# Performance work log

Hardware: AMD Instinct MI355X
Metric: run time of the kernel (lower is better)

Reference implementation:

```python
import jax, jax.numpy as jnp
import numpy as np

D_MODEL = 1024
N_HEADS = 16
D_HEAD = D_MODEL // N_HEADS
B, L = 4, 2048
NEG_INF = float('-inf')


def setup_inputs() -> dict:
    key = jax.random.key(0)
    ks = jax.random.split(key, 8)
    x = jax.random.normal(ks[0], (B, L, D_MODEL), dtype=jnp.float32)
    # sorted cumulative event times in hours (~0-2000h span)
    timestamps = jnp.cumsum(jax.random.uniform(ks[1], (B, L), dtype=jnp.float32), axis=-1)
    mask = jnp.ones((B, L), dtype=jnp.float32)
    s = 1.0 / np.sqrt(D_MODEL)
    W_qkv = jax.random.normal(ks[2], (3 * D_MODEL, D_MODEL), dtype=jnp.float32) * s
    b_qkv = jnp.zeros((3 * D_MODEL,), dtype=jnp.float32)
    W_out = jax.random.normal(ks[3], (D_MODEL, D_MODEL), dtype=jnp.float32) * s
    b_out = jnp.zeros((D_MODEL,), dtype=jnp.float32)
    decay_rate = jnp.full((N_HEADS,), 0.01, dtype=jnp.float32)
    return {"x": x, "timestamps": timestamps, "mask": mask,
            "W_qkv": W_qkv, "b_qkv": b_qkv, "W_out": W_out, "b_out": b_out,
            "decay_rate": decay_rate}


def reference(x, timestamps, mask, W_qkv, b_qkv, W_out, b_out, decay_rate):
    Bb, Ll, Dd = x.shape
    H, dh = N_HEADS, D_HEAD
    scale = dh ** (-0.5)
    qkv = x @ W_qkv.T + b_qkv                     # (B,L,3D)
    qkv = qkv.reshape(Bb, Ll, 3, H, dh).transpose(2, 0, 3, 1, 4)  # (3,B,H,L,dh)
    q, k, v = qkv[0], qkv[1], qkv[2]
    attn = jnp.einsum('bhqd,bhkd->bhqk', q, k) * scale
    t_diff = jnp.abs(timestamps[:, :, None] - timestamps[:, None, :])[:, None]  # (B,1,L,L)
    decay = jax.nn.softplus(decay_rate)[None, :, None, None]                    # (1,H,1,1)
    attn = attn - decay * t_diff / 24.0
    causal = jnp.triu(jnp.ones((Ll, Ll), dtype=bool), k=1)        # (L,L) True above diag
    attn = jnp.where(causal[None, None], NEG_INF, attn)
    pad = (mask == 0.0)[:, None, None, :]                         # (B,1,1,L) True=pad key
    attn = jnp.where(pad, NEG_INF, attn)
    attn = jax.nn.softmax(attn, axis=-1)
    out = jnp.einsum('bhqk,bhkd->bhqd', attn, v)                  # (B,H,L,dh)
    out = out.transpose(0, 2, 1, 3).reshape(Bb, Ll, Dd)
    return out @ W_out.T + b_out
```

## Files before the change

### kernel.cpp

```cpp
#include <hip/hip_runtime.h>
#include <stdint.h>
#include <math.h>

#define B_   4
#define L_   2048
#define H_   16
#define DH_  64
#define DM_  1024

typedef __bf16 bf16;
typedef __attribute__((ext_vector_type(8))) __bf16 bf16x8;
typedef __attribute__((ext_vector_type(4))) float f32x4;
typedef __attribute__((ext_vector_type(4))) int i32x4;
typedef __attribute__((ext_vector_type(4))) short s16x4;
typedef unsigned short u16;
typedef unsigned int u32;
typedef __attribute__((ext_vector_type(2))) unsigned int u32x2;
typedef __attribute__((ext_vector_type(4))) unsigned short u16x4;

typedef unsigned int u32g __attribute__((address_space(1)));
typedef unsigned int u32l __attribute__((address_space(3)));

__device__ __forceinline__ u16 f2bf(float f) {
  return __builtin_bit_cast(u16, (bf16)f);
}

__device__ __forceinline__ float exp2_fast(float x) {
  float r; asm("v_exp_f32 %0, %1" : "=v"(r) : "v"(x)); return r;
}

__device__ __forceinline__ void gload16(const void* g, void* l) {
  __builtin_amdgcn_global_load_lds((const u32g*)g, (u32l*)l, 16, 0, 0);
}

__device__ __forceinline__ f32x4 mfma16(s16x4 a, s16x4 b, f32x4 c) {
#if __has_builtin(__builtin_amdgcn_mfma_f32_16x16x16bf16_1k)
  return __builtin_amdgcn_mfma_f32_16x16x16bf16_1k(a, b, c, 0, 0, 0);
#else
  asm volatile("v_mfma_f32_16x16x16_bf16 %0, %1, %2, %0\n\ts_nop 7\n\ts_nop 2"
               : "+v"(c) : "v"(a), "v"(b));
  return c;
#endif
}

__global__ __launch_bounds__(256) void cvt_f32_bf16(const float* __restrict__ src,
                                                    u16* __restrict__ dst, int n4) {
  int i = blockIdx.x * 256 + threadIdx.x;
  if (i >= n4) return;
  f32x4 v = ((const f32x4*)src)[i];
  u16x4 o;
  o[0] = f2bf(v[0]); o[1] = f2bf(v[1]); o[2] = f2bf(v[2]); o[3] = f2bf(v[3]);
  ((u16x4*)dst)[i] = o;
}

__global__ __launch_bounds__(256) void bias_fill(const float* __restrict__ ts,
                                                 const float* __restrict__ msk,
                                                 const float* __restrict__ decay,
                                                 float* __restrict__ Bk) {
  int i = blockIdx.x * 256 + threadIdx.x;
  int bh = i >> 11, l = i & (L_ - 1);
  int b = bh >> 4, h = bh & 15;
  float dc24 = log1pf(__expf(decay[h])) * (1.0f / 24.0f) * 1.44269504f;
  float tv = ts[b * L_ + l], mv = msk[b * L_ + l];
  Bk[i] = (mv != 0.f) ? dc24 * tv : -INFINITY;
}

__global__ __launch_bounds__(256) void gemm_bf16(
    const u16* __restrict__ A, const u16* __restrict__ Bm, const float* __restrict__ bias,
    int M, int N, int K, int mode,
    u16* __restrict__ Qb, u16* __restrict__ Kb, u16* __restrict__ Vt, float* __restrict__ Cout)
{
  extern __shared__ char smem[];
  u16* ltr = (u16*)smem;

  const int tid = threadIdx.x;
  const int m0 = blockIdx.y * 128, n0 = blockIdx.x * 128;
  const int lane = tid & 63, w = tid >> 6;
  const int g = lane >> 4, col = lane & 15;
  const int wr = w >> 1, wc = w & 1;

  f32x4 acc[4][4];
#pragma unroll
  for (int mt = 0; mt < 4; ++mt)
#pragma unroll
    for (int nt = 0; nt < 4; ++nt) {
      acc[mt][nt][0] = 0.f; acc[mt][nt][1] = 0.f;
      acc[mt][nt][2] = 0.f; acc[mt][nt][3] = 0.f;
    }

  auto STAGEG = [&](int k0, int nb) {
    char* dA = smem + (nb << 14);
    char* dB = dA + 8192;
#pragma unroll
    for (int hh = 0; hh < 2; ++hh) {
      int c = tid + hh * 256;
      int row = c >> 2, sub = c & 3;
      int sc = sub ^ ((row >> 1) & 3);
      gload16(A  + (size_t)(m0 + row) * K + (k0 + sc * 8), dA + c * 16);
      gload16(Bm + (size_t)(n0 + row) * K + (k0 + sc * 8), dB + c * 16);
    }
  };

  STAGEG(0, 0);
  __syncthreads();

  const int nk = K >> 5;
  for (int i = 0; i < nk; ++i) {
    const int cur = i & 1;
    if (i + 1 < nk) STAGEG((i + 1) * 32, cur ^ 1);

    const char* bufA = smem + (cur << 14);
    const char* bufB = bufA + 8192;
    bf16x8 af[4], bfr[4];
#pragma unroll
    for (int mt = 0; mt < 4; ++mt) {
      int row = wr * 64 + mt * 16 + col;
      af[mt] = *(const bf16x8*)(bufA + row * 64 + ((g ^ ((row >> 1) & 3)) << 4));
    }
#pragma unroll
    for (int nt = 0; nt < 4; ++nt) {
      int row = wc * 64 + nt * 16 + col;
      bfr[nt] = *(const bf16x8*)(bufB + row * 64 + ((g ^ ((row >> 1) & 3)) << 4));
    }
#pragma unroll
    for (int mt = 0; mt < 4; ++mt)
#pragma unroll
      for (int nt = 0; nt < 4; ++nt)
        acc[mt][nt] = __builtin_amdgcn_mfma_f32_16x16x32_bf16(af[mt], bfr[nt], acc[mt][nt], 0, 0, 0);

    __syncthreads();
  }

  if (mode == 1) {
#pragma unroll
    for (int nt = 0; nt < 4; ++nt) {
      int gn = n0 + wc * 64 + nt * 16 + col;
      float bv = bias[gn];
#pragma unroll
      for (int mt = 0; mt < 4; ++mt) {
        int mbase = m0 + wr * 64 + mt * 16 + g * 4;
#pragma unroll
        for (int r = 0; r < 4; ++r)
          Cout[(size_t)(mbase + r) * N + gn] = acc[mt][nt][r] + bv;
      }
    }
    return;
  }

  const int type = n0 >> 10;
  const float qsc = (type == 0) ? 0.125f * 1.44269504f : 1.0f;
#pragma unroll
  for (int nt = 0; nt < 4; ++nt) {
    int nn = wc * 64 + nt * 16 + col;
    float bv = bias[n0 + nn];
#pragma unroll
    for (int mt = 0; mt < 4; ++mt) {
      int mm = wr * 64 + mt * 16 + g * 4;
#pragma unroll
      for (int r = 0; r < 4; ++r) {
        u16 hv = f2bf((acc[mt][nt][r] + bv) * qsc);
        if (type < 2) ltr[(mm + r) * 136 + nn] = hv;
        else          ltr[nn * 136 + (mm + r)] = hv;
      }
    }
  }
  __syncthreads();
#pragma unroll
  for (int it = 0; it < 8; ++it) {
    int cid = tid + it * 256;
    int rrow = cid >> 4, cc = cid & 15;
    i32x4 v = *(const i32x4*)((const char*)ltr + rrow * 272 + cc * 16);
    if (type < 2) {
      int token = m0 + rrow;
      int bb = token >> 11, ll = token & (L_ - 1);
      int gn = n0 + cc * 8;
      int head = (gn & 1023) >> 6, d = gn & 63;
      u16* dst = (type == 0) ? Qb : Kb;
      *(i32x4*)(dst + ((size_t)((bb * H_ + head) * L_ + ll)) * 64 + d) = v;
    } else {
      int gn = n0 + rrow;
      int head = (gn & 1023) >> 6, d = gn & 63;
      int token0 = m0 + cc * 8;
      int bb = token0 >> 11, ll = token0 & (L_ - 1);
      *(i32x4*)(Vt + ((size_t)((bb * H_ + head) * DH_ + d)) * L_ + ll) = v;
    }
  }
}

__global__ __launch_bounds__(512, 2) void attn_fwd(
    const u16* __restrict__ Qb, const u16* __restrict__ Kb, const u16* __restrict__ Vt,
    const float* __restrict__ Bk, u16* __restrict__ AO)
{
  __shared__ u16 lK[2][64 * 64];
  __shared__ u16 lV[2][64 * 64];

  const int phys = blockIdx.x;
  const int xcd = phys & 7, s = phys >> 3;
  const int bh = xcd * 8 + (s >> 3);
  const int pr = s & 7;
  const int qa = pr, qbt = 15 - pr;
  const int b = bh >> 4, h = bh & 15;

  const int tid = threadIdx.x, w = tid >> 6, lane = tid & 63;
  const int g = lane >> 4, q16 = lane & 15;

  const float* Bkb = Bk + (size_t)bh * L_;

  int kcol[2], vcol[4];
#pragma unroll
  for (int kk = 0; kk < 2; ++kk) kcol[kk] = ((kk * 4 + g) ^ (q16 & 7)) << 4;
#pragma unroll
  for (int t = 0; t < 4; ++t)
    vcol[t] = (((2 * t + (g >> 1)) ^ (q16 & 7)) << 4) + (g & 1) * 8;

  const int nkA = (qa + 1) * 2;
  const int nkB = (qbt + 1) * 2;

  auto STAGE = [&](int kt, int nb) {
    const int kg0 = kt * 64;
    const int r8 = tid >> 3, cc = tid & 7;
    gload16(Kb + ((size_t)bh * L_ + kg0 + r8) * 64 + ((cc ^ (r8 & 7)) * 8),
            (char*)lK[nb] + tid * 16);
    gload16(Vt + ((size_t)(bh * 64 + r8)) * L_ + kg0 + ((cc ^ (r8 & 7)) * 8),
            (char*)lV[nb] + tid * 16);
  };

  auto BODY = [&](bf16x8 (&qf)[2], f32x4 (&o)[4], float& m_r, float& l_r,
                  int qrow, int kg0, int cur) {
    f32x4 bk[4];
#pragma unroll
    for (int t = 0; t < 4; ++t)
      bk[t] = *(const f32x4*)(Bkb + kg0 + t * 16 + g * 4);

    f32x4 sv[4];
#pragma unroll
    for (int t = 0; t < 4; ++t) { sv[t][0] = 0.f; sv[t][1] = 0.f; sv[t][2] = 0.f; sv[t][3] = 0.f; }
    __builtin_amdgcn_s_setprio(1);
#pragma unroll
    for (int t = 0; t < 4; ++t) {
      const char* krow = (const char*)lK[cur] + t * 2048 + q16 * 128;
#pragma unroll
      for (int kk = 0; kk < 2; ++kk) {
        bf16x8 kf = *(const bf16x8*)(krow + kcol[kk]);
        sv[t] = __builtin_amdgcn_mfma_f32_16x16x32_bf16(kf, qf[kk], sv[t], 0, 0, 0);
      }
    }
    __builtin_amdgcn_s_setprio(0);

#pragma unroll
    for (int t = 0; t < 4; ++t) {
      sv[t][0] += bk[t][0]; sv[t][1] += bk[t][1];
      sv[t][2] += bk[t][2]; sv[t][3] += bk[t][3];
    }

    if (kg0 + 63 > qrow) {
      const int qg = qrow + q16;
#pragma unroll
      for (int t = 0; t < 4; ++t)
#pragma unroll
        for (int r = 0; r < 4; ++r)
          sv[t][r] = (kg0 + t * 16 + g * 4 + r <= qg) ? sv[t][r] : -INFINITY;
    }

    float mx = sv[0][0];
#pragma unroll
    for (int t = 0; t < 4; ++t)
#pragma unroll
      for (int r = 0; r < 4; ++r) mx = fmaxf(mx, sv[t][r]);
    mx = fmaxf(mx, __shfl_xor(mx, 16));
    mx = fmaxf(mx, __shfl_xor(mx, 32));

    float mn = m_r;
    if (__any(mx > m_r + 8.f)) {
      mn = fmaxf(m_r, mx);
      float al = exp2_fast(m_r - mn);
      m_r = mn;
      l_r *= al;
#pragma unroll
      for (int db = 0; db < 4; ++db) {
        o[db][0] *= al; o[db][1] *= al; o[db][2] *= al; o[db][3] *= al;
      }
    }
    float rs = 0.f;
#pragma unroll
    for (int t = 0; t < 4; ++t)
#pragma unroll
      for (int r = 0; r < 4; ++r) {
        float pv = exp2_fast(sv[t][r] - mn);
        sv[t][r] = pv;
        rs += pv;
      }
    l_r += rs;

    s16x4 pf[4];
#pragma unroll
    for (int t = 0; t < 4; ++t) {
      s16x4 pp;
      pp[0] = (short)f2bf(sv[t][0]); pp[1] = (short)f2bf(sv[t][1]);
      pp[2] = (short)f2bf(sv[t][2]); pp[3] = (short)f2bf(sv[t][3]);
      pf[t] = pp;
    }

    __builtin_amdgcn_s_setprio(1);
#pragma unroll
    for (int t = 0; t < 4; ++t) {
      const char* vrow = (const char*)lV[cur] + q16 * 128 + vcol[t];
#pragma unroll
      for (int db = 0; db < 4; ++db) {
        s16x4 vf = *(const s16x4*)(vrow + db * 2048);
        o[db] = mfma16(vf, pf[t], o[db]);
      }
    }
    __builtin_amdgcn_s_setprio(0);
  };

  auto EPI = [&](f32x4 (&o)[4], float l_r, int qt) {
    float lt = l_r + __shfl_xor(l_r, 16);
    lt += __shfl_xor(lt, 32);
    float inv = 1.f / lt;
    u16* dst = AO + ((size_t)(b * L_ + qt * 128 + w * 16 + q16)) * DM_ + h * 64 + g * 4;
#pragma unroll
    for (int db = 0; db < 4; ++db) {
      u32x2 pk;
      pk[0] = (u32)f2bf(o[db][0] * inv) | ((u32)f2bf(o[db][1] * inv) << 16);
      pk[1] = (u32)f2bf(o[db][2] * inv) | ((u32)f2bf(o[db][3] * inv) << 16);
      *(u32x2*)(dst + db * 16) = pk;
    }
  };

  STAGE(0, 0);
  __syncthreads();

  {
    const int qrow = qa * 128 + w * 16;
    const int mkt = (qrow + 79) >> 6;
    bf16x8 qf[2];
    {
      const u16* Qr = Qb + ((size_t)bh * L_ + qrow + q16) * 64;
      qf[0] = *(const bf16x8*)(Qr + g * 8);
      qf[1] = *(const bf16x8*)(Qr + 32 + g * 8);
    }
    float m_r = -INFINITY, l_r = 0.f;
    f32x4 o[4];
#pragma unroll
    for (int db = 0; db < 4; ++db) {
      o[db][0] = 0.f; o[db][1] = 0.f; o[db][2] = 0.f; o[db][3] = 0.f;
    }
    for (int st = 0; st < nkA; ++st) {
      const int cur = st & 1;
      if (st + 1 < nkA) STAGE(st + 1, cur ^ 1);
      else              STAGE(0, cur ^ 1);
      if (st < mkt) BODY(qf, o, m_r, l_r, qrow, st * 64, cur);
      __syncthreads();
    }
    EPI(o, l_r, qa);
  }

  {
    const int qrow = qbt * 128 + w * 16;
    const int mkt = (qrow + 79) >> 6;
    bf16x8 qf[2];
    {
      const u16* Qr = Qb + ((size_t)bh * L_ + qrow + q16) * 64;
      qf[0] = *(const bf16x8*)(Qr + g * 8);
      qf[1] = *(const bf16x8*)(Qr + 32 + g * 8);
    }
    float m_r = -INFINITY, l_r = 0.f;
    f32x4 o[4];
#pragma unroll
    for (int db = 0; db < 4; ++db) {
      o[db][0] = 0.f; o[db][1] = 0.f; o[db][2] = 0.f; o[db][3] = 0.f;
    }
    for (int kt = 0; kt < nkB; ++kt) {
      const int cur = kt & 1;
      if (kt + 1 < nkB) STAGE(kt + 1, cur ^ 1);
      if (kt < mkt) BODY(qf, o, m_r, l_r, qrow, kt * 64, cur);
      __syncthreads();
    }
    EPI(o, l_r, qbt);
  }
}

extern "C" void kernel_launch(void* const* d_in, const int* in_sizes, int n_in,
                              void* d_out, int out_size, void* d_ws, size_t ws_size,
                              hipStream_t stream) {
  const float* x    = (const float*)d_in[0];
  const float* ts   = (const float*)d_in[1];
  const float* mk   = (const float*)d_in[2];
  const float* Wqkv = (const float*)d_in[3];
  const float* bqkv = (const float*)d_in[4];
  const float* Wout = (const float*)d_in[5];
  const float* bout = (const float*)d_in[6];
  const float* dec  = (const float*)d_in[7];
  float* out = (float*)d_out;

  char* ws = (char*)d_ws;
  u16* xbf  = (u16*)(ws + 0);
  u16* wqbf = (u16*)(ws + 16777216);
  u16* wobf = (u16*)(ws + 23068672);
  u16* Qb   = (u16*)(ws + 25165824);
  u16* Kb   = (u16*)(ws + 41943040);
  u16* Vt   = (u16*)(ws + 58720256);
  u16* AO   = (u16*)(ws + 75497472);
  float* Bk = (float*)(ws + 92274688);

  cvt_f32_bf16<<<dim3(8192 * 1024 / 4 / 256), 256, 0, stream>>>(x, xbf, 8192 * 1024 / 4);
  cvt_f32_bf16<<<dim3(3072 * 1024 / 4 / 256), 256, 0, stream>>>(Wqkv, wqbf, 3072 * 1024 / 4);
  cvt_f32_bf16<<<dim3(1024 * 1024 / 4 / 256), 256, 0, stream>>>(Wout, wobf, 1024 * 1024 / 4);

  bias_fill<<<dim3(64 * 2048 / 256), 256, 0, stream>>>(ts, mk, dec, Bk);

  gemm_bf16<<<dim3(3072 / 128, 8192 / 128), 256, 34816, stream>>>(
      xbf, wqbf, bqkv, 8192, 3072, 1024, 0, Qb, Kb, Vt, nullptr);

  attn_fwd<<<dim3(512), 512, 0, stream>>>(Qb, Kb, Vt, Bk, AO);

  gemm_bf16<<<dim3(1024 / 128, 8192 / 128), 256, 32768, stream>>>(
      AO, wobf, bout, 8192, 1024, 1024, 1, nullptr, nullptr, nullptr, out);
}
```

Before: 196.8 us.

## Triple-buffer K/V tiles in attention with explicit vmcnt waits

Moves the attention kernel's K/V shared-memory staging from double to triple buffering. Prefetch now runs two tiles ahead, using a global stage index that spans both query tiles, so the loads for the second tile overlap the end of the first. __syncthreads is replaced by explicit s_waitcnt vmcnt(2) plus s_barrier, so only the oldest tile's loads must land. The bias is also loaded straight into the MFMA accumulator and the max reduction is rebalanced. This costs 50% more LDS per block, which may hurt occupancy at two blocks per CU.

Result: no change. 194.0 us (-1.4%).

```diff
diff --git a/kernel.cpp b/kernel.cpp
--- a/kernel.cpp
+++ b/kernel.cpp
@@ -191,8 +191,8 @@
     const u16* __restrict__ Qb, const u16* __restrict__ Kb, const u16* __restrict__ Vt,
     const float* __restrict__ Bk, u16* __restrict__ AO)
 {
-  __shared__ u16 lK[2][64 * 64];
-  __shared__ u16 lV[2][64 * 64];
+  __shared__ u16 lK[3][64 * 64];
+  __shared__ u16 lV[3][64 * 64];
 
   const int phys = blockIdx.x;
   const int xcd = phys & 7, s = phys >> 3;
@@ -216,7 +216,8 @@
   const int nkA = (qa + 1) * 2;
   const int nkB = (qbt + 1) * 2;
 
-  auto STAGE = [&](int kt, int nb) {
+  auto STAGE = [&](int gst, int nb) {
+    const int kt = (gst < nkA) ? gst : gst - nkA;
     const int kg0 = kt * 64;
     const int r8 = tid >> 3, cc = tid & 7;
     gload16(Kb + ((size_t)bh * L_ + kg0 + r8) * 64 + ((cc ^ (r8 & 7)) * 8),
@@ -227,14 +228,11 @@
 
   auto BODY = [&](bf16x8 (&qf)[2], f32x4 (&o)[4], float& m_r, float& l_r,
                   int qrow, int kg0, int cur) {
-    f32x4 bk[4];
+    f32x4 sv[4];
 #pragma unroll
     for (int t = 0; t < 4; ++t)
-      bk[t] = *(const f32x4*)(Bkb + kg0 + t * 16 + g * 4);
-
-    f32x4 sv[4];
-#pragma unroll
-    for (int t = 0; t < 4; ++t) { sv[t][0] = 0.f; sv[t][1] = 0.f; sv[t][2] = 0.f; sv[t][3] = 0.f; }
+      sv[t] = *(const f32x4*)(Bkb + kg0 + t * 16 + g * 4);
+
     __builtin_amdgcn_s_setprio(1);
 #pragma unroll
     for (int t = 0; t < 4; ++t) {
@@ -247,12 +245,6 @@
     }
     __builtin_amdgcn_s_setprio(0);
 
-#pragma unroll
-    for (int t = 0; t < 4; ++t) {
-      sv[t][0] += bk[t][0]; sv[t][1] += bk[t][1];
-      sv[t][2] += bk[t][2]; sv[t][3] += bk[t][3];
-    }
-
     if (kg0 + 63 > qrow) {
       const int qg = qrow + q16;
 #pragma unroll
@@ -262,11 +254,13 @@
           sv[t][r] = (kg0 + t * 16 + g * 4 + r <= qg) ? sv[t][r] : -INFINITY;
     }
 
-    float mx = sv[0][0];
-#pragma unroll
-    for (int t = 0; t < 4; ++t)
-#pragma unroll
-      for (int r = 0; r < 4; ++r) mx = fmaxf(mx, sv[t][r]);
+    float mx = fmaxf(sv[0][0], sv[0][1]);
+    mx = fmaxf(mx, fmaxf(sv[0][2], sv[0][3]));
+#pragma unroll
+    for (int t = 1; t < 4; ++t) {
+      mx = fmaxf(mx, fmaxf(sv[t][0], sv[t][1]));
+      mx = fmaxf(mx, fmaxf(sv[t][2], sv[t][3]));
+    }
     mx = fmaxf(mx, __shfl_xor(mx, 16));
     mx = fmaxf(mx, __shfl_xor(mx, 32));
 
@@ -329,7 +323,10 @@
   };
 
   STAGE(0, 0);
-  __syncthreads();
+  STAGE(1, 1);
+  asm volatile("s_waitcnt vmcnt(2) lgkmcnt(0)" ::: "memory");
+  __builtin_amdgcn_s_barrier();
+  __builtin_amdgcn_sched_barrier(0);
 
   {
     const int qrow = qa * 128 + w * 16;
@@ -347,11 +344,12 @@
       o[db][0] = 0.f; o[db][1] = 0.f; o[db][2] = 0.f; o[db][3] = 0.f;
     }
     for (int st = 0; st < nkA; ++st) {
-      const int cur = st & 1;
-      if (st + 1 < nkA) STAGE(st + 1, cur ^ 1);
-      else              STAGE(0, cur ^ 1);
+      const int cur = st % 3;
+      STAGE(st + 2, (st + 2) % 3);
       if (st < mkt) BODY(qf, o, m_r, l_r, qrow, st * 64, cur);
-      __syncthreads();
+      asm volatile("s_waitcnt vmcnt(2) lgkmcnt(0)" ::: "memory");
+      __builtin_amdgcn_s_barrier();
+      __builtin_amdgcn_sched_barrier(0);
     }
     EPI(o, l_r, qa);
   }
@@ -372,10 +370,17 @@
       o[db][0] = 0.f; o[db][1] = 0.f; o[db][2] = 0.f; o[db][3] = 0.f;
     }
     for (int kt = 0; kt < nkB; ++kt) {
-      const int cur = kt & 1;
-      if (kt + 1 < nkB) STAGE(kt + 1, cur ^ 1);
+      const int gst = nkA + kt;
+      const int cur = gst % 3;
+      const bool pf = (kt + 2 < nkB);
+      if (pf) STAGE(gst + 2, (gst + 2) % 3);
       if (kt < mkt) BODY(qf, o, m_r, l_r, qrow, kt * 64, cur);
-      __syncthreads();
+      if (kt + 1 < nkB) {
+        if (pf) asm volatile("s_waitcnt vmcnt(2) lgkmcnt(0)" ::: "memory");
+        else    asm volatile("s_waitcnt vmcnt(0) lgkmcnt(0)" ::: "memory");
+        __builtin_amdgcn_s_barrier();
+        __builtin_amdgcn_sched_barrier(0);
+      }
     }
     EPI(o, l_r, qbt);
   }
```
